# Optimization experiments

Hardware: AMD Instinct MI355X
Metric: run time of the kernel (lower is better)

The kernel has to match this reference:

```python
import jax, jax.numpy as jnp
import numpy as np

B, T, DIN, D = 8, 2048, 512, 1024
LN_EPS = 1e-5


def setup_inputs() -> dict:
    key = jax.random.key(0)
    ks = jax.random.split(key, 4)
    x = jax.random.normal(ks[0], (B, T, DIN), dtype=jnp.float32)
    Wd = jax.random.normal(ks[1], (DIN, D), dtype=jnp.float32) * (1.0 / np.sqrt(DIN))
    bd = jnp.zeros((D,), jnp.float32)  # nn.init.constant_(delta_proj.bias, 0)
    Wb = jax.random.normal(ks[2], (DIN, D), dtype=jnp.float32) * (1.0 / np.sqrt(DIN))
    bb = jax.random.normal(ks[3], (D,), dtype=jnp.float32) * 0.02
    A_log = jnp.log(jnp.linspace(1.0, 16.0, D, dtype=jnp.float32))
    threshold = jnp.ones((D,), jnp.float32)
    gamma = jnp.ones((D,), jnp.float32)
    beta = jnp.zeros((D,), jnp.float32)
    return {"x": x, "Wd": Wd, "bd": bd, "Wb": Wb, "bb": bb,
            "A_log": A_log, "threshold": threshold, "gamma": gamma, "beta": beta}


def reference(x, Wd, bd, Wb, bb, A_log, threshold, gamma, beta):
    # Input-dependent discretization (parallel over B,T)
    delta = jax.nn.softplus(jnp.einsum('btc,cd->btd', x, Wd) + bd)   # [B,T,D]
    b_step = delta * (jnp.einsum('btc,cd->btd', x, Wb) + bb)          # [B,T,D]
    A = jnp.exp(A_log)                                                # [D]
    a_step = jnp.exp(-delta * A)                                      # [B,T,D]

    # Sequential spiking scan with multiplicative threshold reset (fp32)
    def step(h, ab):
        a, b = ab
        h = a * h + b
        s = (h - threshold > 0).astype(h.dtype)  # spike (no grad path)
        h = h * (1.0 - s)                        # reset
        return h, (h, s)

    aT = jnp.swapaxes(a_step, 0, 1)  # [T,B,D]
    bT = jnp.swapaxes(b_step, 0, 1)
    h0 = jnp.zeros((x.shape[0], A.shape[0]), a_step.dtype)
    _, (hT, sT) = jax.lax.scan(step, h0, (aT, bT))
    h_post = jnp.swapaxes(hT, 0, 1)  # [B,T,D]
    spikes = jnp.swapaxes(sT, 0, 1)

    # LayerNorm over last dim (biased variance, as torch)
    mu = jnp.mean(h_post, axis=-1, keepdims=True)
    var = jnp.mean(jnp.square(h_post - mu), axis=-1, keepdims=True)
    out = (h_post - mu) * jax.lax.rsqrt(var + LN_EPS) * gamma + beta
    return out, spikes
```

## Files before the change

kernel.cpp:

```cpp
#include <hip/hip_runtime.h>
#include <math.h>

#define BB   8
#define TT   2048
#define CIN  512
#define DD   1024
#define MM   (BB * TT)

constexpr int BM = 64;
constexpr int BN = 128;
constexpr int BK = 16;

#define NCHUNK 32
#define CLEN   (TT / NCHUNK)
#define WARM   128

__device__ __forceinline__ float softplus_f(float z) {
    return fmaxf(z, 0.f) + log1pf(expf(-fabsf(z)));
}

__global__ __launch_bounds__(256) void k1_gemm_act(
    const float* __restrict__ x,
    const float* __restrict__ Wd,
    const float* __restrict__ Wb,
    const float* __restrict__ bd,
    const float* __restrict__ bb,
    const float* __restrict__ A_log,
    float* __restrict__ a_out,
    float* __restrict__ b_out)
{
    __shared__ float xs[BK][BM + 4];
    __shared__ float wds[BK][BN];
    __shared__ float wbs[BK][BN];

    const int tid = threadIdx.x;
    const int n0  = blockIdx.x * BN;
    const int m0  = blockIdx.y * BM;
    const int tx  = tid & 15;
    const int ty  = tid >> 4;

    const int lm = tid >> 2;
    const int lk = (tid & 3) * 4;
    const int wr = tid >> 4;
    const int wc = (tid & 15) * 4;

    float accd[4][8], accb[4][8];
#pragma unroll
    for (int r = 0; r < 4; ++r)
#pragma unroll
        for (int c = 0; c < 8; ++c) { accd[r][c] = 0.f; accb[r][c] = 0.f; }

    const float* xp  = x + (size_t)(m0 + lm) * CIN + lk;
    const float* wdp = Wd + (size_t)wr * DD + n0 + wc;
    const float* wbp = Wb + (size_t)wr * DD + n0 + wc;
    float4 xv  = *(const float4*)(xp);
    float4 wd0 = *(const float4*)(wdp);
    float4 wd1 = *(const float4*)(wdp + 64);
    float4 wb0 = *(const float4*)(wbp);
    float4 wb1 = *(const float4*)(wbp + 64);

    for (int k0 = 0; k0 < CIN; k0 += BK) {
        __syncthreads();
        xs[lk + 0][lm] = xv.x;  xs[lk + 1][lm] = xv.y;
        xs[lk + 2][lm] = xv.z;  xs[lk + 3][lm] = xv.w;
        *(float4*)&wds[wr][wc]      = wd0;
        *(float4*)&wds[wr][wc + 64] = wd1;
        *(float4*)&wbs[wr][wc]      = wb0;
        *(float4*)&wbs[wr][wc + 64] = wb1;
        __syncthreads();

        const int kn = k0 + BK;
        if (kn < CIN) {
            xv  = *(const float4*)(xp + kn);
            wd0 = *(const float4*)(wdp + (size_t)kn * DD);
            wd1 = *(const float4*)(wdp + (size_t)kn * DD + 64);
            wb0 = *(const float4*)(wbp + (size_t)kn * DD);
            wb1 = *(const float4*)(wbp + (size_t)kn * DD + 64);
        }

#pragma unroll
        for (int kk = 0; kk < BK; ++kk) {
            float4 xa = *(const float4*)&xs[kk][ty * 4];
            float4 d0 = *(const float4*)&wds[kk][tx * 4];
            float4 d1 = *(const float4*)&wds[kk][64 + tx * 4];
            float4 c0 = *(const float4*)&wbs[kk][tx * 4];
            float4 c1 = *(const float4*)&wbs[kk][64 + tx * 4];
            float xr[4] = {xa.x, xa.y, xa.z, xa.w};
            float wd[8] = {d0.x, d0.y, d0.z, d0.w, d1.x, d1.y, d1.z, d1.w};
            float wb[8] = {c0.x, c0.y, c0.z, c0.w, c1.x, c1.y, c1.z, c1.w};
#pragma unroll
            for (int r = 0; r < 4; ++r) {
                const float xi = xr[r];
#pragma unroll
                for (int c = 0; c < 8; ++c) {
                    accd[r][c] = fmaf(xi, wd[c], accd[r][c]);
                    accb[r][c] = fmaf(xi, wb[c], accb[r][c]);
                }
            }
        }
    }

    const int nc0 = n0 + tx * 4;
    float4 bdq[2], bbq[2], alq[2];
    bdq[0] = *(const float4*)(bd + nc0);      bdq[1] = *(const float4*)(bd + nc0 + 64);
    bbq[0] = *(const float4*)(bb + nc0);      bbq[1] = *(const float4*)(bb + nc0 + 64);
    alq[0] = *(const float4*)(A_log + nc0);   alq[1] = *(const float4*)(A_log + nc0 + 64);
    float Aq[2][4];
#pragma unroll
    for (int q = 0; q < 2; ++q) {
        Aq[q][0] = expf(alq[q].x); Aq[q][1] = expf(alq[q].y);
        Aq[q][2] = expf(alq[q].z); Aq[q][3] = expf(alq[q].w);
    }

#pragma unroll
    for (int r = 0; r < 4; ++r) {
        const int m = m0 + ty * 4 + r;
        float* ap = a_out + (size_t)m * DD + nc0;
        float* bp = b_out + (size_t)m * DD + nc0;
#pragma unroll
        for (int q = 0; q < 2; ++q) {
            const float* bdv = (const float*)&bdq[q];
            const float* bbv = (const float*)&bbq[q];
            float av[4], bv[4];
#pragma unroll
            for (int j = 0; j < 4; ++j) {
                float zd    = accd[r][q * 4 + j] + bdv[j];
                float delta = softplus_f(zd);
                float zb    = accb[r][q * 4 + j] + bbv[j];
                av[j] = expf(-delta * Aq[q][j]);
                bv[j] = delta * zb;
            }
            *(float4*)(ap + q * 64) = make_float4(av[0], av[1], av[2], av[3]);
            *(float4*)(bp + q * 64) = make_float4(bv[0], bv[1], bv[2], bv[3]);
        }
    }
}

__global__ __launch_bounds__(64) void k2_scan(
    const float* __restrict__ a,
    const float* __restrict__ b,
    const float* __restrict__ thr,
    float* __restrict__ hout,
    float* __restrict__ sout)
{
    const int gid   = blockIdx.x * 64 + threadIdx.x;
    const int batch = gid >> 10;
    const int d     = gid & (DD - 1);
    const float th  = thr[d];
    const size_t base = (size_t)batch * TT * DD + d;

    const int chunk = blockIdx.y;
    const int t0    = chunk * CLEN;
    const int tw    = (t0 - WARM > 0) ? (t0 - WARM) : 0;

    const float* ap = a + base + (size_t)tw * DD;
    const float* bp = b + base + (size_t)tw * DD;

    float h = 0.f;
    for (int t = tw; t < t0; ++t) {
        const float av = *ap; const float bv = *bp;
        ap += DD; bp += DD;
        h = fmaf(av, h, bv);
        h = ((h - th) > 0.f) ? 0.f : h;
    }

    float* hp  = hout + base + (size_t)t0 * DD;
    float* spp = sout + base + (size_t)t0 * DD;
#pragma unroll 8
    for (int t = 0; t < CLEN; ++t) {
        const float av = *ap; const float bv = *bp;
        ap += DD; bp += DD;
        h = fmaf(av, h, bv);
        const bool spike = (h - th) > 0.f;
        *spp = spike ? 1.f : 0.f;
        h = spike ? 0.f : h;
        *hp = h;
        hp += DD; spp += DD;
    }
}

__global__ __launch_bounds__(256) void k3_ln(
    float* __restrict__ h,
    const float* __restrict__ gamma,
    const float* __restrict__ beta)
{
    const int row = blockIdx.x;
    const int tid = threadIdx.x;
    const int lane = tid & 63;
    const int wid  = tid >> 6;

    __shared__ float red[4];
    __shared__ float bc[2];

    float* rp = h + (size_t)row * DD + tid * 4;
    float4 v = *(const float4*)rp;

    float s = v.x + v.y + v.z + v.w;
#pragma unroll
    for (int off = 32; off > 0; off >>= 1) s += __shfl_down(s, off);
    if (lane == 0) red[wid] = s;
    __syncthreads();
    if (tid == 0) bc[0] = (red[0] + red[1] + red[2] + red[3]) * (1.0f / DD);
    __syncthreads();
    const float mu = bc[0];

    float dx = v.x - mu, dy = v.y - mu, dz = v.z - mu, dw = v.w - mu;
    float ss = dx * dx + dy * dy + dz * dz + dw * dw;
#pragma unroll
    for (int off = 32; off > 0; off >>= 1) ss += __shfl_down(ss, off);
    __syncthreads();
    if (lane == 0) red[wid] = ss;
    __syncthreads();
    if (tid == 0) bc[1] = (red[0] + red[1] + red[2] + red[3]) * (1.0f / DD);
    __syncthreads();
    const float inv = 1.0f / sqrtf(bc[1] + 1e-5f);

    float4 g  = *(const float4*)(gamma + tid * 4);
    float4 be = *(const float4*)(beta + tid * 4);
    float4 o;
    o.x = dx * inv * g.x + be.x;
    o.y = dy * inv * g.y + be.y;
    o.z = dz * inv * g.z + be.z;
    o.w = dw * inv * g.w + be.w;
    *(float4*)rp = o;
}

extern "C" void kernel_launch(void* const* d_in, const int* in_sizes, int n_in,
                              void* d_out, int out_size, void* d_ws, size_t ws_size,
                              hipStream_t stream) {
    const float* x     = (const float*)d_in[0];
    const float* Wd    = (const float*)d_in[1];
    const float* bd    = (const float*)d_in[2];
    const float* Wb    = (const float*)d_in[3];
    const float* bb    = (const float*)d_in[4];
    const float* A_log = (const float*)d_in[5];
    const float* thr   = (const float*)d_in[6];
    const float* gamma = (const float*)d_in[7];
    const float* beta  = (const float*)d_in[8];

    float* out    = (float*)d_out;
    float* spikes = out + (size_t)MM * DD;
    float* a_ws   = (float*)d_ws;
    float* b_ws   = a_ws + (size_t)MM * DD;

    dim3 g1(DD / BN, MM / BM);
    k1_gemm_act<<<g1, 256, 0, stream>>>(x, Wd, Wb, bd, bb, A_log, a_ws, b_ws);

    dim3 g2(BB * DD / 64, NCHUNK);
    k2_scan<<<g2, 64, 0, stream>>>(a_ws, b_ws, thr, out, spikes);

    k3_ln<<<MM, 256, 0, stream>>>(out, gamma, beta);
}
```

Before: 692.6 us.

## Software-pipeline scan loads in double-buffered register blocks and retile GEMM

```diff
diff --git a/kernel.cpp b/kernel.cpp
--- a/kernel.cpp
+++ b/kernel.cpp
@@ -7,13 +7,14 @@
 #define DD   1024
 #define MM   (BB * TT)
 
-constexpr int BM = 64;
-constexpr int BN = 128;
+constexpr int BM = 128;
+constexpr int BN = 64;
 constexpr int BK = 16;
 
-#define NCHUNK 32
+#define NCHUNK 16
 #define CLEN   (TT / NCHUNK)
 #define WARM   128
+#define PF     16
 
 __device__ __forceinline__ float softplus_f(float z) {
     return fmaxf(z, 0.f) + log1pf(expf(-fabsf(z)));
@@ -39,60 +40,57 @@
     const int tx  = tid & 15;
     const int ty  = tid >> 4;
 
-    const int lm = tid >> 2;
-    const int lk = (tid & 3) * 4;
+    const int lm = tid >> 1;
+    const int lk = (tid & 1) * 8;
     const int wr = tid >> 4;
     const int wc = (tid & 15) * 4;
 
-    float accd[4][8], accb[4][8];
-#pragma unroll
-    for (int r = 0; r < 4; ++r)
-#pragma unroll
-        for (int c = 0; c < 8; ++c) { accd[r][c] = 0.f; accb[r][c] = 0.f; }
+    float accd[8][4], accb[8][4];
+#pragma unroll
+    for (int r = 0; r < 8; ++r)
+#pragma unroll
+        for (int c = 0; c < 4; ++c) { accd[r][c] = 0.f; accb[r][c] = 0.f; }
 
     const float* xp  = x + (size_t)(m0 + lm) * CIN + lk;
     const float* wdp = Wd + (size_t)wr * DD + n0 + wc;
     const float* wbp = Wb + (size_t)wr * DD + n0 + wc;
-    float4 xv  = *(const float4*)(xp);
+    float4 xva = *(const float4*)(xp);
+    float4 xvb = *(const float4*)(xp + 4);
     float4 wd0 = *(const float4*)(wdp);
-    float4 wd1 = *(const float4*)(wdp + 64);
     float4 wb0 = *(const float4*)(wbp);
-    float4 wb1 = *(const float4*)(wbp + 64);
 
     for (int k0 = 0; k0 < CIN; k0 += BK) {
         __syncthreads();
-        xs[lk + 0][lm] = xv.x;  xs[lk + 1][lm] = xv.y;
-        xs[lk + 2][lm] = xv.z;  xs[lk + 3][lm] = xv.w;
-        *(float4*)&wds[wr][wc]      = wd0;
-        *(float4*)&wds[wr][wc + 64] = wd1;
-        *(float4*)&wbs[wr][wc]      = wb0;
-        *(float4*)&wbs[wr][wc + 64] = wb1;
+        xs[lk + 0][lm] = xva.x;  xs[lk + 1][lm] = xva.y;
+        xs[lk + 2][lm] = xva.z;  xs[lk + 3][lm] = xva.w;
+        xs[lk + 4][lm] = xvb.x;  xs[lk + 5][lm] = xvb.y;
+        xs[lk + 6][lm] = xvb.z;  xs[lk + 7][lm] = xvb.w;
+        *(float4*)&wds[wr][wc] = wd0;
+        *(float4*)&wbs[wr][wc] = wb0;
         __syncthreads();
 
         const int kn = k0 + BK;
         if (kn < CIN) {
-            xv  = *(const float4*)(xp + kn);
+            xva = *(const float4*)(xp + kn);
+            xvb = *(const float4*)(xp + kn + 4);
             wd0 = *(const float4*)(wdp + (size_t)kn * DD);
-            wd1 = *(const float4*)(wdp + (size_t)kn * DD + 64);
             wb0 = *(const float4*)(wbp + (size_t)kn * DD);
-            wb1 = *(const float4*)(wbp + (size_t)kn * DD + 64);
         }
 
 #pragma unroll
         for (int kk = 0; kk < BK; ++kk) {
-            float4 xa = *(const float4*)&xs[kk][ty * 4];
-            float4 d0 = *(const float4*)&wds[kk][tx * 4];
-            float4 d1 = *(const float4*)&wds[kk][64 + tx * 4];
-            float4 c0 = *(const float4*)&wbs[kk][tx * 4];
-            float4 c1 = *(const float4*)&wbs[kk][64 + tx * 4];
-            float xr[4] = {xa.x, xa.y, xa.z, xa.w};
-            float wd[8] = {d0.x, d0.y, d0.z, d0.w, d1.x, d1.y, d1.z, d1.w};
-            float wb[8] = {c0.x, c0.y, c0.z, c0.w, c1.x, c1.y, c1.z, c1.w};
-#pragma unroll
-            for (int r = 0; r < 4; ++r) {
+            float4 xa  = *(const float4*)&xs[kk][ty * 8];
+            float4 xa2 = *(const float4*)&xs[kk][ty * 8 + 4];
+            float4 d0  = *(const float4*)&wds[kk][tx * 4];
+            float4 c0  = *(const float4*)&wbs[kk][tx * 4];
+            float xr[8] = {xa.x, xa.y, xa.z, xa.w, xa2.x, xa2.y, xa2.z, xa2.w};
+            float wd[4] = {d0.x, d0.y, d0.z, d0.w};
+            float wb[4] = {c0.x, c0.y, c0.z, c0.w};
+#pragma unroll
+            for (int r = 0; r < 8; ++r) {
                 const float xi = xr[r];
 #pragma unroll
-                for (int c = 0; c < 8; ++c) {
+                for (int c = 0; c < 4; ++c) {
                     accd[r][c] = fmaf(xi, wd[c], accd[r][c]);
                     accb[r][c] = fmaf(xi, wb[c], accb[r][c]);
                 }
@@ -101,38 +99,27 @@
     }
 
     const int nc0 = n0 + tx * 4;
-    float4 bdq[2], bbq[2], alq[2];
-    bdq[0] = *(const float4*)(bd + nc0);      bdq[1] = *(const float4*)(bd + nc0 + 64);
-    bbq[0] = *(const float4*)(bb + nc0);      bbq[1] = *(const float4*)(bb + nc0 + 64);
-    alq[0] = *(const float4*)(A_log + nc0);   alq[1] = *(const float4*)(A_log + nc0 + 64);
-    float Aq[2][4];
-#pragma unroll
-    for (int q = 0; q < 2; ++q) {
-        Aq[q][0] = expf(alq[q].x); Aq[q][1] = expf(alq[q].y);
-        Aq[q][2] = expf(alq[q].z); Aq[q][3] = expf(alq[q].w);
-    }
-
-#pragma unroll
-    for (int r = 0; r < 4; ++r) {
-        const int m = m0 + ty * 4 + r;
-        float* ap = a_out + (size_t)m * DD + nc0;
-        float* bp = b_out + (size_t)m * DD + nc0;
-#pragma unroll
-        for (int q = 0; q < 2; ++q) {
-            const float* bdv = (const float*)&bdq[q];
-            const float* bbv = (const float*)&bbq[q];
-            float av[4], bv[4];
-#pragma unroll
-            for (int j = 0; j < 4; ++j) {
-                float zd    = accd[r][q * 4 + j] + bdv[j];
-                float delta = softplus_f(zd);
-                float zb    = accb[r][q * 4 + j] + bbv[j];
-                av[j] = expf(-delta * Aq[q][j]);
-                bv[j] = delta * zb;
-            }
-            *(float4*)(ap + q * 64) = make_float4(av[0], av[1], av[2], av[3]);
-            *(float4*)(bp + q * 64) = make_float4(bv[0], bv[1], bv[2], bv[3]);
-        }
+    float4 bdq = *(const float4*)(bd + nc0);
+    float4 bbq = *(const float4*)(bb + nc0);
+    float4 alq = *(const float4*)(A_log + nc0);
+    const float* bdv = (const float*)&bdq;
+    const float* bbv = (const float*)&bbq;
+    float Aq[4] = {expf(alq.x), expf(alq.y), expf(alq.z), expf(alq.w)};
+
+#pragma unroll
+    for (int r = 0; r < 8; ++r) {
+        const int m = m0 + ty * 8 + r;
+        float av[4], bv[4];
+#pragma unroll
+        for (int j = 0; j < 4; ++j) {
+            float zd    = accd[r][j] + bdv[j];
+            float delta = softplus_f(zd);
+            float zb    = accb[r][j] + bbv[j];
+            av[j] = expf(-delta * Aq[j]);
+            bv[j] = delta * zb;
+        }
+        *(float4*)(a_out + (size_t)m * DD + nc0) = make_float4(av[0], av[1], av[2], av[3]);
+        *(float4*)(b_out + (size_t)m * DD + nc0) = make_float4(bv[0], bv[1], bv[2], bv[3]);
     }
 }
 
@@ -151,31 +138,68 @@
 
     const int chunk = blockIdx.y;
     const int t0    = chunk * CLEN;
-    const int tw    = (t0 - WARM > 0) ? (t0 - WARM) : 0;
+    const int nwarm = (chunk == 0) ? 0 : WARM;
+    const int tw    = t0 - nwarm;
+    const int nwb   = nwarm / PF;
+    const int ntot  = nwb + CLEN / PF;
 
     const float* ap = a + base + (size_t)tw * DD;
     const float* bp = b + base + (size_t)tw * DD;
+    float* hp = hout + base + (size_t)t0 * DD;
+    float* sp = sout + base + (size_t)t0 * DD;
+
+    float a0[PF], b0[PF], a1[PF], b1[PF];
+#pragma unroll
+    for (int j = 0; j < PF; ++j) { a0[j] = ap[(size_t)j * DD]; b0[j] = bp[(size_t)j * DD]; }
+    ap += (size_t)PF * DD; bp += (size_t)PF * DD;
 
     float h = 0.f;
-    for (int t = tw; t < t0; ++t) {
-        const float av = *ap; const float bv = *bp;
-        ap += DD; bp += DD;
-        h = fmaf(av, h, bv);
-        h = ((h - th) > 0.f) ? 0.f : h;
-    }
-
-    float* hp  = hout + base + (size_t)t0 * DD;
-    float* spp = sout + base + (size_t)t0 * DD;
-#pragma unroll 8
-    for (int t = 0; t < CLEN; ++t) {
-        const float av = *ap; const float bv = *bp;
-        ap += DD; bp += DD;
-        h = fmaf(av, h, bv);
-        const bool spike = (h - th) > 0.f;
-        *spp = spike ? 1.f : 0.f;
-        h = spike ? 0.f : h;
-        *hp = h;
-        hp += DD; spp += DD;
+    for (int i = 0; i < ntot; i += 2) {
+#pragma unroll
+        for (int j = 0; j < PF; ++j) { a1[j] = ap[(size_t)j * DD]; b1[j] = bp[(size_t)j * DD]; }
+        ap += (size_t)PF * DD; bp += (size_t)PF * DD;
+
+        if (i >= nwb) {
+#pragma unroll
+            for (int j = 0; j < PF; ++j) {
+                h = fmaf(a0[j], h, b0[j]);
+                const bool spike = (h - th) > 0.f;
+                *sp = spike ? 1.f : 0.f;
+                h = spike ? 0.f : h;
+                *hp = h;
+                hp += DD; sp += DD;
+            }
+        } else {
+#pragma unroll
+            for (int j = 0; j < PF; ++j) {
+                h = fmaf(a0[j], h, b0[j]);
+                h = ((h - th) > 0.f) ? 0.f : h;
+            }
+        }
+
+        if (i + 2 < ntot) {
+#pragma unroll
+            for (int j = 0; j < PF; ++j) { a0[j] = ap[(size_t)j * DD]; b0[j] = bp[(size_t)j * DD]; }
+            ap += (size_t)PF * DD; bp += (size_t)PF * DD;
+        }
+
+        if (i + 1 >= nwb) {
+#pragma unroll
+            for (int j = 0; j < PF; ++j) {
+                h = fmaf(a1[j], h, b1[j]);
+                const bool spike = (h - th) > 0.f;
+                *sp = spike ? 1.f : 0.f;
+                h = spike ? 0.f : h;
+                *hp = h;
+                hp += DD; sp += DD;
+            }
+        } else {
+#pragma unroll
+            for (int j = 0; j < PF; ++j) {
+                h = fmaf(a1[j], h, b1[j]);
+                h = ((h - th) > 0.f) ? 0.f : h;
+            }
+        }
     }
 }
 
```

Result: no change. 684.2 us (-1.2%).
